# Performance work log

Hardware: AMD Instinct MI355X
Metric: run time of the kernel (lower is better)

The kernel has to match this reference:

```python
import jax, jax.numpy as jnp
import numpy as np

N = 50000   # nodes
E = 1600000 # edges
K = 5       # Chebyshev order
F_IN, H1, H2, P = 32, 32, 16, 12


def setup_inputs() -> dict:
    key = jax.random.key(0)
    ks = jax.random.split(key, 16)
    x = jax.random.normal(ks[0], (N, F_IN), dtype=jnp.float32)
    edge_index = jax.random.randint(ks[1], (2, E), 0, N, dtype=jnp.int64)
    edge_weight = jax.random.uniform(ks[2], (E,), dtype=jnp.float32)
    s = 0.1
    # Cell 1: 3 gates (z, r, h), each with x-conv [K,F_IN,H1] and h-conv [K,H1,H1]
    Wx1 = jax.random.normal(ks[3], (3, K, F_IN, H1), dtype=jnp.float32) * s
    bx1 = jax.random.normal(ks[4], (3, H1), dtype=jnp.float32) * s
    Wh1 = jax.random.normal(ks[5], (3, K, H1, H1), dtype=jnp.float32) * s
    bh1 = jax.random.normal(ks[6], (3, H1), dtype=jnp.float32) * s
    # Cell 2
    Wx2 = jax.random.normal(ks[7], (3, K, H1, H2), dtype=jnp.float32) * s
    bx2 = jax.random.normal(ks[8], (3, H2), dtype=jnp.float32) * s
    Wh2 = jax.random.normal(ks[9], (3, K, H2, H2), dtype=jnp.float32) * s
    bh2 = jax.random.normal(ks[10], (3, H2), dtype=jnp.float32) * s
    # Output linear (torch convention: weight [out,in])
    Wl = jax.random.normal(ks[11], (P, H2), dtype=jnp.float32) * s
    bl = jax.random.normal(ks[12], (P,), dtype=jnp.float32) * s
    return dict(x=x, edge_index=edge_index, edge_weight=edge_weight,
                Wx1=Wx1, bx1=bx1, Wh1=Wh1, bh1=bh1,
                Wx2=Wx2, bx2=bx2, Wh2=Wh2, bh2=bh2, Wl=Wl, bl=bl)


def _cheb_norm(edge_index, edge_weight):
    # ChebConv 'sym' norm with lambda_max=2: L_hat off-diagonal = -D^-1/2 A D^-1/2,
    # diagonal cancels to 0 (get_laplacian +1 self loop, add_self_loops fill -1).
    row, col = edge_index[0], edge_index[1]
    deg = jax.ops.segment_sum(edge_weight, row, num_segments=N)
    dis = jnp.where(deg > 0, jax.lax.rsqrt(jnp.maximum(deg, 1e-30)), 0.0)
    return -dis[row] * edge_weight * dis[col]


def _gconv_gru_forward(x, edge_index, edge_weight, Wx1, bx1, Wh1, bh1,
                       Wx2, bx2, Wh2, bh2, Wl, bl):
    row, col = edge_index[0], edge_index[1]
    wn = _cheb_norm(edge_index, edge_weight)

    def spmm(v):  # (L_hat @ v): gather source rows, scatter-add to targets
        return jax.ops.segment_sum(v[row] * wn[:, None], col, num_segments=N)

    def cheb(v, W, b):  # W: [K, Fin, Fout]
        Tx0 = v
        out = Tx0 @ W[0]
        Tx1 = spmm(Tx0)
        out = out + Tx1 @ W[1]
        for k in range(2, K):
            Tx2 = 2.0 * spmm(Tx1) - Tx0
            out = out + Tx2 @ W[k]
            Tx0, Tx1 = Tx1, Tx2
        return out + b

    def gru_cell(v, H, Wx, bx, Wh, bh):
        Z = jax.nn.sigmoid(cheb(v, Wx[0], bx[0]) + cheb(H, Wh[0], bh[0]))
        R = jax.nn.sigmoid(cheb(v, Wx[1], bx[1]) + cheb(H, Wh[1], bh[1]))
        Ht = jnp.tanh(cheb(v, Wx[2], bx[2]) + cheb(H * R, Wh[2], bh[2]))
        return Z * H + (1.0 - Z) * Ht

    h = gru_cell(x, jnp.zeros((N, H1), x.dtype), Wx1, bx1, Wh1, bh1)
    h = jax.nn.relu(h)  # dropout is identity in eval mode
    h = gru_cell(h, jnp.zeros((N, H2), x.dtype), Wx2, bx2, Wh2, bh2)
    h = jax.nn.relu(h)
    return h @ Wl.T + bl


def reference(x, edge_index, edge_weight, Wx1, bx1, Wh1, bh1,
              Wx2, bx2, Wh2, bh2, Wl, bl):
    return _gconv_gru_forward(x, edge_index, edge_weight, Wx1, bx1, Wh1, bh1,
                              Wx2, bx2, Wh2, bh2, Wl, bl)
```

## Files before the change

### kernel.cpp

```cpp
#include <hip/hip_runtime.h>
#include <math.h>

#define NN 50000
#define NE 1600000
#define KORD 5
#define NB 196
#define QTR 12500
#define GE 782
#define MT 64
#define NBK 1563
#define NBP 1600
#define NCH 256
#define ECH (NE / NCH)
#define EC4 (NE / 64)
#define PADE 1800192
#define CVB 1563

#define SCALE_W 2097152.0f
#define INV_SCALE_W (1.0f / 2097152.0f)
#define SCALE_D 4194304.0f
#define INV_SCALE_D (1.0f / 4194304.0f)

typedef _Float16 half8 __attribute__((ext_vector_type(8)));
typedef _Float16 half4v __attribute__((ext_vector_type(4)));
typedef float float4v __attribute__((ext_vector_type(4)));

__global__ __launch_bounds__(1024) void k_degbh(const int* __restrict__ ei,
                                                const float* __restrict__ ew,
                                                int* __restrict__ deg_g,
                                                int* __restrict__ bh) {
    __shared__ int sbuf[QTR];
    int bid = blockIdx.x;
    if (bid < 256) {
        int q = bid >> 6, ch = bid & 63;
        for (int i = threadIdx.x; i < QTR; i += 1024) sbuf[i] = 0;
        __syncthreads();
        int base = ch * EC4, lo = q * QTR;
        for (int e = base + threadIdx.x; e < base + EC4; e += 1024) {
            int li = ei[e] - lo;
            if ((unsigned)li < (unsigned)QTR)
                atomicAdd(&sbuf[li], __float2int_rn(ew[e] * SCALE_D));
        }
        __syncthreads();
        int* outp = deg_g + bid * QTR;
        for (int i = threadIdx.x; i < QTR; i += 1024) outp[i] = sbuf[i];
    } else {
        int ch = bid - 256;
        for (int i = threadIdx.x; i < NBK; i += 1024) sbuf[i] = 0;
        __syncthreads();
        const int* cols = ei + NE;
        int base = ch * ECH;
        for (int e = base + threadIdx.x; e < base + ECH; e += 1024)
            atomicAdd(&sbuf[cols[e] >> 5], 1);
        __syncthreads();
        int* outp = bh + ch * NBP;
        for (int b = threadIdx.x; b < NBK; b += 1024) outp[b] = sbuf[b];
    }
}

__global__ __launch_bounds__(256) void k_btotdiscvt(const int* __restrict__ bh,
                                                    int* __restrict__ tot,
                                                    const int* __restrict__ deg_g,
                                                    float* __restrict__ dis,
                                                    const float* __restrict__ x,
                                                    _Float16* __restrict__ x16) {
    int bid = blockIdx.x;
    if (bid < 7) {
        int b = bid * 256 + threadIdx.x;
        if (b >= NBP) return;
        int s = 0;
        if (b < NBK) {
#pragma unroll 8
            for (int ch = 0; ch < NCH; ch++) s += bh[ch * NBP + b];
        }
        tot[b] = s;
    } else if (bid < 7 + NB) {
        int n = (bid - 7) * 256 + threadIdx.x;
        if (n >= NN) return;
        int q = n / QTR, i = n % QTR;
        const int* p = deg_g + (q * 64) * QTR + i;
        int s = 0;
#pragma unroll
        for (int c = 0; c < 64; c++) s += p[c * QTR];
        float d = (float)s * INV_SCALE_D;
        dis[n] = s > 0 ? rsqrtf(fmaxf(d, 1e-30f)) : 0.f;
    } else {
        int i = (bid - 7 - NB) * 256 + threadIdx.x;
        if (i < NN * 8) {
            float4 v = ((const float4*)x)[i];
            half4v h = {(_Float16)v.x, (_Float16)v.y, (_Float16)v.z, (_Float16)v.w};
            *(half4v*)(x16 + i * 4) = h;
        }
    }
}

__global__ __launch_bounds__(1024) void k_bscan1(const int* __restrict__ tot,
                                                 int* __restrict__ off_bk) {
    __shared__ int s[1024];
    int t = threadIdx.x;
    int a0 = (2 * t < NBP) ? tot[2 * t] : 0;
    int a1 = (2 * t + 1 < NBP) ? tot[2 * t + 1] : 0;
    int p0 = (a0 + 127) & ~127;
    int p1 = (a1 + 127) & ~127;
    s[t] = p0 + p1;
    __syncthreads();
    for (int d = 1; d < 1024; d <<= 1) {
        int u = (t >= d) ? s[t - d] : 0;
        __syncthreads();
        s[t] += u;
        __syncthreads();
    }
    int excl = (t == 0) ? 0 : s[t - 1];
    if (2 * t < NBK) off_bk[2 * t] = excl;
    if (2 * t + 1 < NBK) off_bk[2 * t + 1] = excl + p0;
    if (t == 1023) off_bk[NBK] = s[1023];
}

__global__ __launch_bounds__(256) void k_curpad(int* __restrict__ bh,
                                                const int* __restrict__ off_bk,
                                                const int* __restrict__ tot,
                                                int2* __restrict__ edges) {
    int bid = blockIdx.x;
    if (bid < 7) {
        int b = bid * 256 + threadIdx.x;
        if (b >= NBK) return;
        int run = off_bk[b];
        for (int ch = 0; ch < NCH; ch++) {
            int v = bh[ch * NBP + b];
            bh[ch * NBP + b] = run;
            run += v;
        }
    } else {
        int b = bid - 7;
        int start = off_bk[b] + tot[b];
        int end = off_bk[b + 1];
        for (int i = start + threadIdx.x; i < end; i += 256)
            edges[i] = make_int2(0, 0);
    }
}

__global__ __launch_bounds__(1024) void k_cperm(const int* __restrict__ ei,
                                                const float* __restrict__ ew,
                                                const float* __restrict__ dis,
                                                const int* __restrict__ bh,
                                                int2* __restrict__ edges) {
    __shared__ int cur[NBK];
    int ch = blockIdx.x;
    const int* cp = bh + ch * NBP;
    for (int b = threadIdx.x; b < NBK; b += 1024) cur[b] = cp[b];
    __syncthreads();
    int base = ch * ECH;
    for (int e = base + threadIdx.x; e < base + ECH; e += 1024) {
        int r = ei[e], c = ei[NE + e];
        float w = -dis[r] * ew[e] * dis[c];
        int pos = atomicAdd(&cur[c >> 5], 1);
        int packed = (int)((unsigned)r | ((unsigned)(c & 31) << 16));
        edges[pos] = make_int2(packed, __float_as_int(w));
    }
}

#define SPMM_DS2(C0, W0, G0, C1, W1, G1)                       \
    {                                                          \
        int* a0 = &acc[C0][sub * 8];                           \
        int* a1 = &acc[C1][sub * 8];                           \
        atomicAdd(a0 + 0, __float2int_rn(W0 * (float)G0[0]));  \
        atomicAdd(a0 + 1, __float2int_rn(W0 * (float)G0[1]));  \
        atomicAdd(a0 + 2, __float2int_rn(W0 * (float)G0[2]));  \
        atomicAdd(a0 + 3, __float2int_rn(W0 * (float)G0[3]));  \
        atomicAdd(a0 + 4, __float2int_rn(W0 * (float)G0[4]));  \
        atomicAdd(a0 + 5, __float2int_rn(W0 * (float)G0[5]));  \
        atomicAdd(a0 + 6, __float2int_rn(W0 * (float)G0[6]));  \
        atomicAdd(a0 + 7, __float2int_rn(W0 * (float)G0[7]));  \
        atomicAdd(a1 + 0, __float2int_rn(W1 * (float)G1[0]));  \
        atomicAdd(a1 + 1, __float2int_rn(W1 * (float)G1[1]));  \
        atomicAdd(a1 + 2, __float2int_rn(W1 * (float)G1[2]));  \
        atomicAdd(a1 + 3, __float2int_rn(W1 * (float)G1[3]));  \
        atomicAdd(a1 + 4, __float2int_rn(W1 * (float)G1[4]));  \
        atomicAdd(a1 + 5, __float2int_rn(W1 * (float)G1[5]));  \
        atomicAdd(a1 + 6, __float2int_rn(W1 * (float)G1[6]));  \
        atomicAdd(a1 + 7, __float2int_rn(W1 * (float)G1[7]));  \
    }

__global__ __launch_bounds__(256) void k_spmm(const int* __restrict__ off_bk,
                                              const int2* __restrict__ edges,
                                              const _Float16* __restrict__ vin16,
                                              const float* __restrict__ prev,
                                              float* __restrict__ vout,
                                              _Float16* __restrict__ vout16,
                                              float scale) {
    __shared__ int acc[32][33];
    int b = blockIdx.x;
    {
        int nl = threadIdx.x >> 3, s4 = threadIdx.x & 7;
        int n = (b << 5) + nl;
        float4 p = make_float4(0.f, 0.f, 0.f, 0.f);
        if (prev && n < NN) p = ((const float4*)prev)[n * 8 + s4];
        int* a = &acc[nl][s4 * 4];
        a[0] = __float2int_rn(-p.x * SCALE_W);
        a[1] = __float2int_rn(-p.y * SCALE_W);
        a[2] = __float2int_rn(-p.z * SCALE_W);
        a[3] = __float2int_rn(-p.w * SCALE_W);
    }
    __syncthreads();
    int e0 = off_bk[b], e1 = off_bk[b + 1];
    int group = threadIdx.x >> 2, sub = threadIdx.x & 3;
    const half8* vin8 = (const half8*)vin16;
    float wscale = scale * SCALE_W;
    int nit = (e1 - e0) >> 7;
    if (nit > 0) {
        int i = e0 + group;
        int2 Ra0 = edges[i], Ra1 = edges[i + 64];
        int2 Rb0 = make_int2(0, 0), Rb1 = make_int2(0, 0);
        int2 Rc0 = make_int2(0, 0), Rc1 = make_int2(0, 0);
        if (nit > 1) { Rb0 = edges[i + 128]; Rb1 = edges[i + 192]; }
        if (nit > 2) { Rc0 = edges[i + 256]; Rc1 = edges[i + 320]; }
        half8 Ga0 = vin8[((unsigned)Ra0.x & 0xffffu) * 4 + sub];
        half8 Ga1 = vin8[((unsigned)Ra1.x & 0xffffu) * 4 + sub];
        half8 Gb0 = {}, Gb1 = {};
        if (nit > 1) {
            Gb0 = vin8[((unsigned)Rb0.x & 0xffffu) * 4 + sub];
            Gb1 = vin8[((unsigned)Rb1.x & 0xffffu) * 4 + sub];
        }
        for (int k = 0; k < nit; k++) {
            int2 Rd0 = make_int2(0, 0), Rd1 = make_int2(0, 0);
            if (k + 3 < nit) { Rd0 = edges[i + 384]; Rd1 = edges[i + 448]; }
            half8 Gc0 = {}, Gc1 = {};
            if (k + 2 < nit) {
                Gc0 = vin8[((unsigned)Rc0.x & 0xffffu) * 4 + sub];
                Gc1 = vin8[((unsigned)Rc1.x & 0xffffu) * 4 + sub];
            }
            int C0 = (unsigned)Ra0.x >> 16, C1 = (unsigned)Ra1.x >> 16;
            float W0 = __int_as_float(Ra0.y) * wscale;
            float W1 = __int_as_float(Ra1.y) * wscale;
            SPMM_DS2(C0, W0, Ga0, C1, W1, Ga1);
            Ra0 = Rb0; Ra1 = Rb1; Rb0 = Rc0; Rb1 = Rc1; Rc0 = Rd0; Rc1 = Rd1;
            Ga0 = Gb0; Ga1 = Gb1; Gb0 = Gc0; Gb1 = Gc1;
            i += 128;
        }
    }
    __syncthreads();
    int base = b << 5;
    int nl = threadIdx.x >> 3, s4 = threadIdx.x & 7;
    int n = base + nl;
    if (n < NN) {
        const int* a = &acc[nl][s4 * 4];
        float4 o = make_float4((float)a[0] * INV_SCALE_W, (float)a[1] * INV_SCALE_W,
                               (float)a[2] * INV_SCALE_W, (float)a[3] * INV_SCALE_W);
        if (vout) ((float4*)vout)[n * 8 + s4] = o;
        half4v oh = {(_Float16)o.x, (_Float16)o.y, (_Float16)o.z, (_Float16)o.w};
        *(half4v*)(vout16 + n * 32 + s4 * 4) = oh;
    }
}

__global__ __launch_bounds__(256) void k_epi1(
    const _Float16* __restrict__ x16, const _Float16* __restrict__ t1,
    const _Float16* __restrict__ t2, const _Float16* __restrict__ t3,
    const _Float16* __restrict__ t4, const float* __restrict__ Wx1,
    const float* __restrict__ bx1, const float* __restrict__ bh1,
    float* __restrict__ h, _Float16* __restrict__ h16) {
    __shared__ _Float16 T[5][MT][40];
    __shared__ _Float16 Wt[64][168];
    int n0 = blockIdx.x * MT;
    const _Float16* bufs[5] = {x16, t1, t2, t3, t4};
#pragma unroll
    for (int b = 0; b < 5; b++) {
        for (int idx = threadIdx.x; idx < MT * 4; idx += 256) {
            int r = idx >> 2, c8 = idx & 3;
            int rr = n0 + r; if (rr >= NN) rr = NN - 1;
            half8 v = *(const half8*)(bufs[b] + rr * 32 + c8 * 8);
            *(half8*)&T[b][r][c8 * 8] = v;
        }
    }
    const float* Wz = Wx1;
    const float* Wh = Wx1 + 2 * KORD * 32 * 32;
    for (int idx = threadIdx.x; idx < 160 * 64; idx += 256) {
        int k = idx >> 6, n = idx & 63;
        int b = k >> 5, i = k & 31;
        float w = (n < 32) ? Wz[b * 1024 + i * 32 + n]
                           : Wh[b * 1024 + i * 32 + (n - 32)];
        Wt[n][k] = (_Float16)w;
    }
    __syncthreads();
    int wave = threadIdx.x >> 6;
    int lane = threadIdx.x & 63;
    int lo = lane & 15, quad = lane >> 4;
    float4v acc[4];
#pragma unroll
    for (int t = 0; t < 4; t++) acc[t] = (float4v){0.f, 0.f, 0.f, 0.f};
#pragma unroll
    for (int b = 0; b < 5; b++) {
        half8 a = *(half8*)&T[b][wave * 16 + lo][quad * 8];
#pragma unroll
        for (int t = 0; t < 4; t++) {
            half8 bf = *(half8*)&Wt[t * 16 + lo][b * 32 + quad * 8];
            acc[t] = __builtin_amdgcn_mfma_f32_16x16x32_f16(a, bf, acc[t], 0, 0, 0);
        }
    }
    int nd_base = n0 + wave * 16 + quad * 4;
#pragma unroll
    for (int t = 0; t < 2; t++) {
        int j = t * 16 + lo;
        float bz = bx1[j] + bh1[j];
        float bhb = bx1[64 + j] + bh1[64 + j];
#pragma unroll
        for (int reg = 0; reg < 4; reg++) {
            int nd = nd_base + reg;
            if (nd < NN) {
                float zz = acc[t][reg] + bz;
                float hh = acc[t + 2][reg] + bhb;
                float z = 1.f / (1.f + __expf(-zz));
                float tt = __expf(-2.f * fabsf(hh));
                float ht = copysignf((1.f - tt) / (1.f + tt), hh);
                float v = fmaxf((1.f - z) * ht, 0.f);
                h[nd * 32 + j] = v;
                h16[nd * 32 + j] = (_Float16)v;
            }
        }
    }
}

__global__ __launch_bounds__(256) void k_epi2(
    const _Float16* __restrict__ h16, const _Float16* __restrict__ t1,
    const _Float16* __restrict__ t2, const _Float16* __restrict__ t3,
    const _Float16* __restrict__ t4, const float* __restrict__ Wx2,
    const float* __restrict__ bx2, const float* __restrict__ bh2,
    const float* __restrict__ Wl, const float* __restrict__ bl,
    float* __restrict__ out) {
    __shared__ _Float16 T[5][MT][40];
    __shared__ _Float16 Wt[32][168];
    __shared__ float H2[MT][17];
    int n0 = blockIdx.x * MT;
    const _Float16* bufs[5] = {h16, t1, t2, t3, t4};
#pragma unroll
    for (int b = 0; b < 5; b++) {
        for (int idx = threadIdx.x; idx < MT * 4; idx += 256) {
            int r = idx >> 2, c8 = idx & 3;
            int rr = n0 + r; if (rr >= NN) rr = NN - 1;
            half8 v = *(const half8*)(bufs[b] + rr * 32 + c8 * 8);
            *(half8*)&T[b][r][c8 * 8] = v;
        }
    }
    const float* Wz = Wx2;
    const float* Wh = Wx2 + 2 * KORD * 32 * 16;
    for (int idx = threadIdx.x; idx < 160 * 32; idx += 256) {
        int k = idx >> 5, n = idx & 31;
        int b = k >> 5, i = k & 31;
        float w = (n < 16) ? Wz[b * 512 + i * 16 + n]
                           : Wh[b * 512 + i * 16 + (n - 16)];
        Wt[n][k] = (_Float16)w;
    }
    __syncthreads();
    int wave = threadIdx.x >> 6;
    int lane = threadIdx.x & 63;
    int lo = lane & 15, quad = lane >> 4;
    float4v acc[2];
    acc[0] = (float4v){0.f, 0.f, 0.f, 0.f};
    acc[1] = (float4v){0.f, 0.f, 0.f, 0.f};
#pragma unroll
    for (int b = 0; b < 5; b++) {
        half8 a = *(half8*)&T[b][wave * 16 + lo][quad * 8];
#pragma unroll
        for (int t = 0; t < 2; t++) {
            half8 bf = *(half8*)&Wt[t * 16 + lo][b * 32 + quad * 8];
            acc[t] = __builtin_amdgcn_mfma_f32_16x16x32_f16(a, bf, acc[t], 0, 0, 0);
        }
    }
    {
        int j = lo;
        float bz = bx2[j] + bh2[j];
        float bhb = bx2[32 + j] + bh2[32 + j];
        int ndl_base = wave * 16 + quad * 4;
#pragma unroll
        for (int reg = 0; reg < 4; reg++) {
            float zz = acc[0][reg] + bz;
            float hh = acc[1][reg] + bhb;
            float z = 1.f / (1.f + __expf(-zz));
            float tt = __expf(-2.f * fabsf(hh));
            float ht = copysignf((1.f - tt) / (1.f + tt), hh);
            H2[ndl_base + reg][j] = fmaxf((1.f - z) * ht, 0.f);
        }
    }
    __syncthreads();
    for (int idx = threadIdx.x; idx < MT * 12; idx += 256) {
        int n = idx / 12, p = idx % 12;
        int gn = n0 + n;
        if (gn < NN) {
            float o = bl[p];
#pragma unroll
            for (int jj = 0; jj < 16; jj++) o = fmaf(H2[n][jj], Wl[p * 16 + jj], o);
            out[gn * 12 + p] = o;
        }
    }
}


extern "C" void kernel_launch(void* const* d_in, const int* in_sizes, int n_in,
                              void* d_out, int out_size, void* d_ws, size_t ws_size,
                              hipStream_t stream) {
    const float* x   = (const float*)d_in[0];
    const int*   ei  = (const int*)d_in[1];
    const float* ew  = (const float*)d_in[2];
    const float* Wx1 = (const float*)d_in[3];
    const float* bx1 = (const float*)d_in[4];
    const float* bh1 = (const float*)d_in[6];
    const float* Wx2 = (const float*)d_in[7];
    const float* bx2 = (const float*)d_in[8];
    const float* bh2 = (const float*)d_in[10];
    const float* Wl  = (const float*)d_in[11];
    const float* bl  = (const float*)d_in[12];
    float* out = (float*)d_out;

    float* ws     = (float*)d_ws;
    float* dis    = ws;
    int*   bh     = (int*)(ws + 50048);
    int*   tot    = bh + NCH * NBP;
    int*   off_bk = tot + NBP;
    int2*  edges  = (int2*)(off_bk + NBP);
    float* T1     = (float*)(edges + PADE);
    float* T2     = T1 + NN * 32;
    float* T3     = T2 + NN * 32;
    float* hb     = T3 + NN * 32;
    _Float16* x16 = (_Float16*)(hb + NN * 32);
    _Float16* t1h = x16 + NN * 32;
    _Float16* t2h = t1h + NN * 32;
    _Float16* t3h = t2h + NN * 32;
    _Float16* t4h = t3h + NN * 32;
    _Float16* hbh = t4h + NN * 32;
    int*   deg_g  = (int*)T1;

    k_degbh     <<<512, 1024, 0, stream>>>(ei, ew, deg_g, bh);
    k_btotdiscvt<<<7 + NB + CVB, 256, 0, stream>>>(bh, tot, deg_g, dis, x, x16);
    k_bscan1    <<<1, 1024, 0, stream>>>(tot, off_bk);
    k_curpad    <<<7 + NBK, 256, 0, stream>>>(bh, off_bk, tot, edges);
    k_cperm     <<<NCH, 1024, 0, stream>>>(ei, ew, dis, bh, edges);

    k_spmm<<<NBK, 256, 0, stream>>>(off_bk, edges, x16, nullptr, T1, t1h, 1.f);
    k_spmm<<<NBK, 256, 0, stream>>>(off_bk, edges, t1h, x,      T2, t2h, 2.f);
    k_spmm<<<NBK, 256, 0, stream>>>(off_bk, edges, t2h, T1, nullptr, t3h, 2.f);
    k_spmm<<<NBK, 256, 0, stream>>>(off_bk, edges, t3h, T2, nullptr, t4h, 2.f);
    k_epi1<<<GE, 256, 0, stream>>>(x16, t1h, t2h, t3h, t4h, Wx1, bx1, bh1, hb, hbh);

    k_spmm<<<NBK, 256, 0, stream>>>(off_bk, edges, hbh, nullptr, T1, t1h, 1.f);
    k_spmm<<<NBK, 256, 0, stream>>>(off_bk, edges, t1h, hb,     T2, t2h, 2.f);
    k_spmm<<<NBK, 256, 0, stream>>>(off_bk, edges, t2h, T1, nullptr, t3h, 2.f);
    k_spmm<<<NBK, 256, 0, stream>>>(off_bk, edges, t3h, T2, nullptr, t4h, 2.f);
    k_epi2<<<GE, 256, 0, stream>>>(hbh, t1h, t2h, t3h, t4h, Wx2, bx2, bh2, Wl, bl, out);
}
```

Before: 340.0 us.

## Fuse four Chebyshev SpMM passes into one cooperative kernel with grid syncs

Replaces the four separate k_spmm launches per GRU cell with a single cooperative kernel that runs the four propagation passes back to back, separated by grid-wide barriers, over a persistent grid of 1024 blocks striding across the 1563 node blocks. This removes three kernel launch gaps and tail drains per cell. In exchange, the grid-sync cost is paid each pass, work per pass is less evenly spread (some blocks handle two node blocks, others one), and the launch depends on 1024 blocks being co-resident.

Result: slower. 1.120 ms (+229.3%).

```diff
diff --git a/kernel.cpp b/kernel.cpp
--- a/kernel.cpp
+++ b/kernel.cpp
@@ -1,5 +1,8 @@
 #include <hip/hip_runtime.h>
+#include <hip/hip_cooperative_groups.h>
 #include <math.h>
+
+namespace cg = cooperative_groups;
 
 #define NN 50000
 #define NE 1600000
@@ -15,6 +18,7 @@
 #define EC4 (NE / 64)
 #define PADE 1800192
 #define CVB 1563
+#define GRID_SP 1024
 
 #define SCALE_W 2097152.0f
 #define INV_SCALE_W (1.0f / 2097152.0f)
@@ -181,75 +185,96 @@
         atomicAdd(a1 + 7, __float2int_rn(W1 * (float)G1[7]));  \
     }
 
-__global__ __launch_bounds__(256) void k_spmm(const int* __restrict__ off_bk,
-                                              const int2* __restrict__ edges,
-                                              const _Float16* __restrict__ vin16,
-                                              const float* __restrict__ prev,
-                                              float* __restrict__ vout,
-                                              _Float16* __restrict__ vout16,
-                                              float scale) {
-    __shared__ int acc[32][33];
-    int b = blockIdx.x;
-    {
-        int nl = threadIdx.x >> 3, s4 = threadIdx.x & 7;
-        int n = (b << 5) + nl;
-        float4 p = make_float4(0.f, 0.f, 0.f, 0.f);
-        if (prev && n < NN) p = ((const float4*)prev)[n * 8 + s4];
-        int* a = &acc[nl][s4 * 4];
-        a[0] = __float2int_rn(-p.x * SCALE_W);
-        a[1] = __float2int_rn(-p.y * SCALE_W);
-        a[2] = __float2int_rn(-p.z * SCALE_W);
-        a[3] = __float2int_rn(-p.w * SCALE_W);
-    }
-    __syncthreads();
-    int e0 = off_bk[b], e1 = off_bk[b + 1];
+__device__ __forceinline__ void spmm_pass(const int* __restrict__ off_bk,
+                                          const int2* __restrict__ edges,
+                                          const _Float16* __restrict__ vin16,
+                                          const float* __restrict__ prev,
+                                          float* __restrict__ vout,
+                                          _Float16* __restrict__ vout16,
+                                          float scale, int acc[32][33]) {
     int group = threadIdx.x >> 2, sub = threadIdx.x & 3;
     const half8* vin8 = (const half8*)vin16;
     float wscale = scale * SCALE_W;
-    int nit = (e1 - e0) >> 7;
-    if (nit > 0) {
-        int i = e0 + group;
-        int2 Ra0 = edges[i], Ra1 = edges[i + 64];
-        int2 Rb0 = make_int2(0, 0), Rb1 = make_int2(0, 0);
-        int2 Rc0 = make_int2(0, 0), Rc1 = make_int2(0, 0);
-        if (nit > 1) { Rb0 = edges[i + 128]; Rb1 = edges[i + 192]; }
-        if (nit > 2) { Rc0 = edges[i + 256]; Rc1 = edges[i + 320]; }
-        half8 Ga0 = vin8[((unsigned)Ra0.x & 0xffffu) * 4 + sub];
-        half8 Ga1 = vin8[((unsigned)Ra1.x & 0xffffu) * 4 + sub];
-        half8 Gb0 = {}, Gb1 = {};
-        if (nit > 1) {
-            Gb0 = vin8[((unsigned)Rb0.x & 0xffffu) * 4 + sub];
-            Gb1 = vin8[((unsigned)Rb1.x & 0xffffu) * 4 + sub];
-        }
-        for (int k = 0; k < nit; k++) {
-            int2 Rd0 = make_int2(0, 0), Rd1 = make_int2(0, 0);
-            if (k + 3 < nit) { Rd0 = edges[i + 384]; Rd1 = edges[i + 448]; }
-            half8 Gc0 = {}, Gc1 = {};
-            if (k + 2 < nit) {
-                Gc0 = vin8[((unsigned)Rc0.x & 0xffffu) * 4 + sub];
-                Gc1 = vin8[((unsigned)Rc1.x & 0xffffu) * 4 + sub];
+    for (int b = blockIdx.x; b < NBK; b += GRID_SP) {
+        {
+            int nl = threadIdx.x >> 3, s4 = threadIdx.x & 7;
+            int n = (b << 5) + nl;
+            float4 p = make_float4(0.f, 0.f, 0.f, 0.f);
+            if (prev && n < NN) p = ((const float4*)prev)[n * 8 + s4];
+            int* a = &acc[nl][s4 * 4];
+            a[0] = __float2int_rn(-p.x * SCALE_W);
+            a[1] = __float2int_rn(-p.y * SCALE_W);
+            a[2] = __float2int_rn(-p.z * SCALE_W);
+            a[3] = __float2int_rn(-p.w * SCALE_W);
+        }
+        __syncthreads();
+        int e0 = off_bk[b], e1 = off_bk[b + 1];
+        int nit = (e1 - e0) >> 7;
+        if (nit > 0) {
+            int i = e0 + group;
+            int2 Ra0 = edges[i], Ra1 = edges[i + 64];
+            int2 Rb0 = make_int2(0, 0), Rb1 = make_int2(0, 0);
+            int2 Rc0 = make_int2(0, 0), Rc1 = make_int2(0, 0);
+            if (nit > 1) { Rb0 = edges[i + 128]; Rb1 = edges[i + 192]; }
+            if (nit > 2) { Rc0 = edges[i + 256]; Rc1 = edges[i + 320]; }
+            half8 Ga0 = vin8[((unsigned)Ra0.x & 0xffffu) * 4 + sub];
+            half8 Ga1 = vin8[((unsigned)Ra1.x & 0xffffu) * 4 + sub];
+            half8 Gb0 = {}, Gb1 = {};
+            if (nit > 1) {
+                Gb0 = vin8[((unsigned)Rb0.x & 0xffffu) * 4 + sub];
+                Gb1 = vin8[((unsigned)Rb1.x & 0xffffu) * 4 + sub];
             }
-            int C0 = (unsigned)Ra0.x >> 16, C1 = (unsigned)Ra1.x >> 16;
-            float W0 = __int_as_float(Ra0.y) * wscale;
-            float W1 = __int_as_float(Ra1.y) * wscale;
-            SPMM_DS2(C0, W0, Ga0, C1, W1, Ga1);
-            Ra0 = Rb0; Ra1 = Rb1; Rb0 = Rc0; Rb1 = Rc1; Rc0 = Rd0; Rc1 = Rd1;
-            Ga0 = Gb0; Ga1 = Gb1; Gb0 = Gc0; Gb1 = Gc1;
-            i += 128;
-        }
-    }
-    __syncthreads();
-    int base = b << 5;
-    int nl = threadIdx.x >> 3, s4 = threadIdx.x & 7;
-    int n = base + nl;
-    if (n < NN) {
-        const int* a = &acc[nl][s4 * 4];
-        float4 o = make_float4((float)a[0] * INV_SCALE_W, (float)a[1] * INV_SCALE_W,
-                               (float)a[2] * INV_SCALE_W, (float)a[3] * INV_SCALE_W);
-        if (vout) ((float4*)vout)[n * 8 + s4] = o;
-        half4v oh = {(_Float16)o.x, (_Float16)o.y, (_Float16)o.z, (_Float16)o.w};
-        *(half4v*)(vout16 + n * 32 + s4 * 4) = oh;
-    }
+            for (int k = 0; k < nit; k++) {
+                int2 Rd0 = make_int2(0, 0), Rd1 = make_int2(0, 0);
+                if (k + 3 < nit) { Rd0 = edges[i + 384]; Rd1 = edges[i + 448]; }
+                half8 Gc0 = {}, Gc1 = {};
+                if (k + 2 < nit) {
+                    Gc0 = vin8[((unsigned)Rc0.x & 0xffffu) * 4 + sub];
+                    Gc1 = vin8[((unsigned)Rc1.x & 0xffffu) * 4 + sub];
+                }
+                int C0 = (unsigned)Ra0.x >> 16, C1 = (unsigned)Ra1.x >> 16;
+                float W0 = __int_as_float(Ra0.y) * wscale;
+                float W1 = __int_as_float(Ra1.y) * wscale;
+                SPMM_DS2(C0, W0, Ga0, C1, W1, Ga1);
+                Ra0 = Rb0; Ra1 = Rb1; Rb0 = Rc0; Rb1 = Rc1; Rc0 = Rd0; Rc1 = Rd1;
+                Ga0 = Gb0; Ga1 = Gb1; Gb0 = Gc0; Gb1 = Gc1;
+                i += 128;
+            }
+        }
+        __syncthreads();
+        {
+            int nl = threadIdx.x >> 3, s4 = threadIdx.x & 7;
+            int n = (b << 5) + nl;
+            if (n < NN) {
+                const int* a = &acc[nl][s4 * 4];
+                float4 o = make_float4((float)a[0] * INV_SCALE_W,
+                                       (float)a[1] * INV_SCALE_W,
+                                       (float)a[2] * INV_SCALE_W,
+                                       (float)a[3] * INV_SCALE_W);
+                if (vout) ((float4*)vout)[n * 8 + s4] = o;
+                half4v oh = {(_Float16)o.x, (_Float16)o.y, (_Float16)o.z, (_Float16)o.w};
+                *(half4v*)(vout16 + n * 32 + s4 * 4) = oh;
+            }
+        }
+        __syncthreads();
+    }
+}
+
+__global__ __launch_bounds__(256) void k_spmm4(
+    const int* __restrict__ off_bk, const int2* __restrict__ edges,
+    const _Float16* __restrict__ v0h, const float* __restrict__ v0f,
+    float* __restrict__ T1, float* __restrict__ T2,
+    _Float16* __restrict__ t1h, _Float16* __restrict__ t2h,
+    _Float16* __restrict__ t3h, _Float16* __restrict__ t4h) {
+    __shared__ int acc[32][33];
+    cg::grid_group grid = cg::this_grid();
+    spmm_pass(off_bk, edges, v0h, nullptr, T1, t1h, 1.f, acc);
+    grid.sync();
+    spmm_pass(off_bk, edges, t1h, v0f, T2, t2h, 2.f, acc);
+    grid.sync();
+    spmm_pass(off_bk, edges, t2h, T1, nullptr, t3h, 2.f, acc);
+    grid.sync();
+    spmm_pass(off_bk, edges, t3h, T2, nullptr, t4h, 2.f, acc);
 }
 
 __global__ __launch_bounds__(256) void k_epi1(
@@ -434,15 +459,26 @@
     k_curpad    <<<7 + NBK, 256, 0, stream>>>(bh, off_bk, tot, edges);
     k_cperm     <<<NCH, 1024, 0, stream>>>(ei, ew, dis, bh, edges);
 
-    k_spmm<<<NBK, 256, 0, stream>>>(off_bk, edges, x16, nullptr, T1, t1h, 1.f);
-    k_spmm<<<NBK, 256, 0, stream>>>(off_bk, edges, t1h, x,      T2, t2h, 2.f);
-    k_spmm<<<NBK, 256, 0, stream>>>(off_bk, edges, t2h, T1, nullptr, t3h, 2.f);
-    k_spmm<<<NBK, 256, 0, stream>>>(off_bk, edges, t3h, T2, nullptr, t4h, 2.f);
+    const int* off_bk_c = off_bk;
+    const int2* edges_c = edges;
+
+    {
+        const _Float16* v0h = x16; const float* v0f = x;
+        void* a1[] = {(void*)&off_bk_c, (void*)&edges_c, (void*)&v0h, (void*)&v0f,
+                      (void*)&T1, (void*)&T2, (void*)&t1h, (void*)&t2h,
+                      (void*)&t3h, (void*)&t4h};
+        hipLaunchCooperativeKernel((void*)k_spmm4, dim3(GRID_SP), dim3(256),
+                                   a1, 0, stream);
+    }
     k_epi1<<<GE, 256, 0, stream>>>(x16, t1h, t2h, t3h, t4h, Wx1, bx1, bh1, hb, hbh);
 
-    k_spmm<<<NBK, 256, 0, stream>>>(off_bk, edges, hbh, nullptr, T1, t1h, 1.f);
-    k_spmm<<<NBK, 256, 0, stream>>>(off_bk, edges, t1h, hb,     T2, t2h, 2.f);
-    k_spmm<<<NBK, 256, 0, stream>>>(off_bk, edges, t2h, T1, nullptr, t3h, 2.f);
-    k_spmm<<<NBK, 256, 0, stream>>>(off_bk, edges, t3h, T2, nullptr, t4h, 2.f);
+    {
+        const _Float16* v0h = hbh; const float* v0f = hb;
+        void* a2[] = {(void*)&off_bk_c, (void*)&edges_c, (void*)&v0h, (void*)&v0f,
+                      (void*)&T1, (void*)&T2, (void*)&t1h, (void*)&t2h,
+                      (void*)&t3h, (void*)&t4h};
+        hipLaunchCooperativeKernel((void*)k_spmm4, dim3(GRID_SP), dim3(256),
+                                   a2, 0, stream);
+    }
     k_epi2<<<GE, 256, 0, stream>>>(hbh, t1h, t2h, t3h, t4h, Wx2, bx2, bh2, Wl, bl, out);
 }
```

## Replace bucketed LDS-atomic SpMM with per-node CSR row gather in registers

Applied to the files above, without the earlier changes.

The 32-node bucket layout with padded edge lists and fixed-point LDS atomic accumulation is replaced by a full per-target-node CSR. Edges are now counted per node, scanned in a single-block kernel and scattered with global atomics on per-node cursors. Each SpMM row is then reduced by 4 lanes in fp32 registers with no shared-memory atomics or int quantisation. This removes atomic contention and one preprocessing kernel, but adds variable per-row loop lengths that cause load imbalance, global atomics in the permutation step, and a shorter prefetch depth.

After: 564.0 us. 65.9% more time.

```diff
diff --git a/kernel.cpp b/kernel.cpp
--- a/kernel.cpp
+++ b/kernel.cpp
@@ -8,16 +8,12 @@
 #define QTR 12500
 #define GE 782
 #define MT 64
-#define NBK 1563
-#define NBP 1600
 #define NCH 256
 #define ECH (NE / NCH)
 #define EC4 (NE / 64)
-#define PADE 1800192
 #define CVB 1563
-
-#define SCALE_W 2097152.0f
-#define INV_SCALE_W (1.0f / 2097152.0f)
+#define NPAD 50048
+
 #define SCALE_D 4194304.0f
 #define INV_SCALE_D (1.0f / 4194304.0f)
 
@@ -25,57 +21,45 @@
 typedef _Float16 half4v __attribute__((ext_vector_type(4)));
 typedef float float4v __attribute__((ext_vector_type(4)));
 
-__global__ __launch_bounds__(1024) void k_degbh(const int* __restrict__ ei,
-                                                const float* __restrict__ ew,
-                                                int* __restrict__ deg_g,
-                                                int* __restrict__ bh) {
+__global__ __launch_bounds__(1024) void k_degcnt(const int* __restrict__ ei,
+                                                 const float* __restrict__ ew,
+                                                 int* __restrict__ deg_g,
+                                                 int* __restrict__ cnt_g) {
     __shared__ int sbuf[QTR];
     int bid = blockIdx.x;
+    int local = bid & 255;
+    int q = local >> 6, ch = local & 63;
+    for (int i = threadIdx.x; i < QTR; i += 1024) sbuf[i] = 0;
+    __syncthreads();
+    int base = ch * EC4, lo = q * QTR;
     if (bid < 256) {
-        int q = bid >> 6, ch = bid & 63;
-        for (int i = threadIdx.x; i < QTR; i += 1024) sbuf[i] = 0;
-        __syncthreads();
-        int base = ch * EC4, lo = q * QTR;
         for (int e = base + threadIdx.x; e < base + EC4; e += 1024) {
             int li = ei[e] - lo;
             if ((unsigned)li < (unsigned)QTR)
                 atomicAdd(&sbuf[li], __float2int_rn(ew[e] * SCALE_D));
         }
-        __syncthreads();
-        int* outp = deg_g + bid * QTR;
-        for (int i = threadIdx.x; i < QTR; i += 1024) outp[i] = sbuf[i];
     } else {
-        int ch = bid - 256;
-        for (int i = threadIdx.x; i < NBK; i += 1024) sbuf[i] = 0;
-        __syncthreads();
         const int* cols = ei + NE;
-        int base = ch * ECH;
-        for (int e = base + threadIdx.x; e < base + ECH; e += 1024)
-            atomicAdd(&sbuf[cols[e] >> 5], 1);
-        __syncthreads();
-        int* outp = bh + ch * NBP;
-        for (int b = threadIdx.x; b < NBK; b += 1024) outp[b] = sbuf[b];
-    }
-}
-
-__global__ __launch_bounds__(256) void k_btotdiscvt(const int* __restrict__ bh,
-                                                    int* __restrict__ tot,
-                                                    const int* __restrict__ deg_g,
-                                                    float* __restrict__ dis,
-                                                    const float* __restrict__ x,
-                                                    _Float16* __restrict__ x16) {
+        for (int e = base + threadIdx.x; e < base + EC4; e += 1024) {
+            int li = cols[e] - lo;
+            if ((unsigned)li < (unsigned)QTR)
+                atomicAdd(&sbuf[li], 1);
+        }
+    }
+    __syncthreads();
+    int* outp = (bid < 256 ? deg_g : cnt_g) + local * QTR;
+    for (int i = threadIdx.x; i < QTR; i += 1024) outp[i] = sbuf[i];
+}
+
+__global__ __launch_bounds__(256) void k_discntcvt(const int* __restrict__ deg_g,
+                                                   const int* __restrict__ cnt_g,
+                                                   float* __restrict__ dis,
+                                                   int* __restrict__ cnt,
+                                                   const float* __restrict__ x,
+                                                   _Float16* __restrict__ x16) {
     int bid = blockIdx.x;
-    if (bid < 7) {
-        int b = bid * 256 + threadIdx.x;
-        if (b >= NBP) return;
-        int s = 0;
-        if (b < NBK) {
-#pragma unroll 8
-            for (int ch = 0; ch < NCH; ch++) s += bh[ch * NBP + b];
-        }
-        tot[b] = s;
-    } else if (bid < 7 + NB) {
-        int n = (bid - 7) * 256 + threadIdx.x;
+    if (bid < NB) {
+        int n = bid * 256 + threadIdx.x;
         if (n >= NN) return;
         int q = n / QTR, i = n % QTR;
         const int* p = deg_g + (q * 64) * QTR + i;
@@ -84,8 +68,17 @@
         for (int c = 0; c < 64; c++) s += p[c * QTR];
         float d = (float)s * INV_SCALE_D;
         dis[n] = s > 0 ? rsqrtf(fmaxf(d, 1e-30f)) : 0.f;
+    } else if (bid < 2 * NB) {
+        int n = (bid - NB) * 256 + threadIdx.x;
+        if (n >= NN) return;
+        int q = n / QTR, i = n % QTR;
+        const int* p = cnt_g + (q * 64) * QTR + i;
+        int s = 0;
+#pragma unroll
+        for (int c = 0; c < 64; c++) s += p[c * QTR];
+        cnt[n] = s;
     } else {
-        int i = (bid - 7 - NB) * 256 + threadIdx.x;
+        int i = (bid - 2 * NB) * 256 + threadIdx.x;
         if (i < NN * 8) {
             float4 v = ((const float4*)x)[i];
             half4v h = {(_Float16)v.x, (_Float16)v.y, (_Float16)v.z, (_Float16)v.w};
@@ -94,15 +87,19 @@
     }
 }
 
-__global__ __launch_bounds__(1024) void k_bscan1(const int* __restrict__ tot,
-                                                 int* __restrict__ off_bk) {
+__global__ __launch_bounds__(1024) void k_scan(const int* __restrict__ cnt,
+                                               int* __restrict__ off,
+                                               int* __restrict__ cur) {
     __shared__ int s[1024];
+    const int CH = 49;
     int t = threadIdx.x;
-    int a0 = (2 * t < NBP) ? tot[2 * t] : 0;
-    int a1 = (2 * t + 1 < NBP) ? tot[2 * t + 1] : 0;
-    int p0 = (a0 + 127) & ~127;
-    int p1 = (a1 + 127) & ~127;
-    s[t] = p0 + p1;
+    int base = t * CH;
+    int sum = 0;
+    for (int i = 0; i < CH; i++) {
+        int idx = base + i;
+        if (idx < NN) sum += cnt[idx];
+    }
+    s[t] = sum;
     __syncthreads();
     for (int d = 1; d < 1024; d <<= 1) {
         int u = (t >= d) ? s[t - d] : 0;
@@ -110,146 +107,78 @@
         s[t] += u;
         __syncthreads();
     }
-    int excl = (t == 0) ? 0 : s[t - 1];
-    if (2 * t < NBK) off_bk[2 * t] = excl;
-    if (2 * t + 1 < NBK) off_bk[2 * t + 1] = excl + p0;
-    if (t == 1023) off_bk[NBK] = s[1023];
-}
-
-__global__ __launch_bounds__(256) void k_curpad(int* __restrict__ bh,
-                                                const int* __restrict__ off_bk,
-                                                const int* __restrict__ tot,
-                                                int2* __restrict__ edges) {
-    int bid = blockIdx.x;
-    if (bid < 7) {
-        int b = bid * 256 + threadIdx.x;
-        if (b >= NBK) return;
-        int run = off_bk[b];
-        for (int ch = 0; ch < NCH; ch++) {
-            int v = bh[ch * NBP + b];
-            bh[ch * NBP + b] = run;
-            run += v;
-        }
-    } else {
-        int b = bid - 7;
-        int start = off_bk[b] + tot[b];
-        int end = off_bk[b + 1];
-        for (int i = start + threadIdx.x; i < end; i += 256)
-            edges[i] = make_int2(0, 0);
-    }
+    int run = (t == 0) ? 0 : s[t - 1];
+    for (int i = 0; i < CH; i++) {
+        int idx = base + i;
+        if (idx < NN) {
+            int c = cnt[idx];
+            off[idx] = run;
+            cur[idx] = run;
+            run += c;
+        }
+    }
+    if (t == 1023) off[NN] = s[1023];
 }
 
 __global__ __launch_bounds__(1024) void k_cperm(const int* __restrict__ ei,
                                                 const float* __restrict__ ew,
                                                 const float* __restrict__ dis,
-                                                const int* __restrict__ bh,
+                                                int* __restrict__ cur,
                                                 int2* __restrict__ edges) {
-    __shared__ int cur[NBK];
     int ch = blockIdx.x;
-    const int* cp = bh + ch * NBP;
-    for (int b = threadIdx.x; b < NBK; b += 1024) cur[b] = cp[b];
-    __syncthreads();
     int base = ch * ECH;
     for (int e = base + threadIdx.x; e < base + ECH; e += 1024) {
         int r = ei[e], c = ei[NE + e];
         float w = -dis[r] * ew[e] * dis[c];
-        int pos = atomicAdd(&cur[c >> 5], 1);
-        int packed = (int)((unsigned)r | ((unsigned)(c & 31) << 16));
-        edges[pos] = make_int2(packed, __float_as_int(w));
-    }
-}
-
-#define SPMM_DS2(C0, W0, G0, C1, W1, G1)                       \
-    {                                                          \
-        int* a0 = &acc[C0][sub * 8];                           \
-        int* a1 = &acc[C1][sub * 8];                           \
-        atomicAdd(a0 + 0, __float2int_rn(W0 * (float)G0[0]));  \
-        atomicAdd(a0 + 1, __float2int_rn(W0 * (float)G0[1]));  \
-        atomicAdd(a0 + 2, __float2int_rn(W0 * (float)G0[2]));  \
-        atomicAdd(a0 + 3, __float2int_rn(W0 * (float)G0[3]));  \
-        atomicAdd(a0 + 4, __float2int_rn(W0 * (float)G0[4]));  \
-        atomicAdd(a0 + 5, __float2int_rn(W0 * (float)G0[5]));  \
-        atomicAdd(a0 + 6, __float2int_rn(W0 * (float)G0[6]));  \
-        atomicAdd(a0 + 7, __float2int_rn(W0 * (float)G0[7]));  \
-        atomicAdd(a1 + 0, __float2int_rn(W1 * (float)G1[0]));  \
-        atomicAdd(a1 + 1, __float2int_rn(W1 * (float)G1[1]));  \
-        atomicAdd(a1 + 2, __float2int_rn(W1 * (float)G1[2]));  \
-        atomicAdd(a1 + 3, __float2int_rn(W1 * (float)G1[3]));  \
-        atomicAdd(a1 + 4, __float2int_rn(W1 * (float)G1[4]));  \
-        atomicAdd(a1 + 5, __float2int_rn(W1 * (float)G1[5]));  \
-        atomicAdd(a1 + 6, __float2int_rn(W1 * (float)G1[6]));  \
-        atomicAdd(a1 + 7, __float2int_rn(W1 * (float)G1[7]));  \
-    }
-
-__global__ __launch_bounds__(256) void k_spmm(const int* __restrict__ off_bk,
+        int pos = atomicAdd(&cur[c], 1);
+        edges[pos] = make_int2(r, __float_as_int(w));
+    }
+}
+
+__global__ __launch_bounds__(256) void k_spmm(const int* __restrict__ off,
                                               const int2* __restrict__ edges,
                                               const _Float16* __restrict__ vin16,
                                               const float* __restrict__ prev,
                                               float* __restrict__ vout,
                                               _Float16* __restrict__ vout16,
                                               float scale) {
-    __shared__ int acc[32][33];
-    int b = blockIdx.x;
-    {
-        int nl = threadIdx.x >> 3, s4 = threadIdx.x & 7;
-        int n = (b << 5) + nl;
-        float4 p = make_float4(0.f, 0.f, 0.f, 0.f);
-        if (prev && n < NN) p = ((const float4*)prev)[n * 8 + s4];
-        int* a = &acc[nl][s4 * 4];
-        a[0] = __float2int_rn(-p.x * SCALE_W);
-        a[1] = __float2int_rn(-p.y * SCALE_W);
-        a[2] = __float2int_rn(-p.z * SCALE_W);
-        a[3] = __float2int_rn(-p.w * SCALE_W);
-    }
-    __syncthreads();
-    int e0 = off_bk[b], e1 = off_bk[b + 1];
     int group = threadIdx.x >> 2, sub = threadIdx.x & 3;
+    int n = blockIdx.x * 64 + group;
+    if (n >= NN) return;
     const half8* vin8 = (const half8*)vin16;
-    float wscale = scale * SCALE_W;
-    int nit = (e1 - e0) >> 7;
-    if (nit > 0) {
-        int i = e0 + group;
-        int2 Ra0 = edges[i], Ra1 = edges[i + 64];
-        int2 Rb0 = make_int2(0, 0), Rb1 = make_int2(0, 0);
-        int2 Rc0 = make_int2(0, 0), Rc1 = make_int2(0, 0);
-        if (nit > 1) { Rb0 = edges[i + 128]; Rb1 = edges[i + 192]; }
-        if (nit > 2) { Rc0 = edges[i + 256]; Rc1 = edges[i + 320]; }
-        half8 Ga0 = vin8[((unsigned)Ra0.x & 0xffffu) * 4 + sub];
-        half8 Ga1 = vin8[((unsigned)Ra1.x & 0xffffu) * 4 + sub];
-        half8 Gb0 = {}, Gb1 = {};
-        if (nit > 1) {
-            Gb0 = vin8[((unsigned)Rb0.x & 0xffffu) * 4 + sub];
-            Gb1 = vin8[((unsigned)Rb1.x & 0xffffu) * 4 + sub];
-        }
-        for (int k = 0; k < nit; k++) {
-            int2 Rd0 = make_int2(0, 0), Rd1 = make_int2(0, 0);
-            if (k + 3 < nit) { Rd0 = edges[i + 384]; Rd1 = edges[i + 448]; }
-            half8 Gc0 = {}, Gc1 = {};
-            if (k + 2 < nit) {
-                Gc0 = vin8[((unsigned)Rc0.x & 0xffffu) * 4 + sub];
-                Gc1 = vin8[((unsigned)Rc1.x & 0xffffu) * 4 + sub];
-            }
-            int C0 = (unsigned)Ra0.x >> 16, C1 = (unsigned)Ra1.x >> 16;
-            float W0 = __int_as_float(Ra0.y) * wscale;
-            float W1 = __int_as_float(Ra1.y) * wscale;
-            SPMM_DS2(C0, W0, Ga0, C1, W1, Ga1);
-            Ra0 = Rb0; Ra1 = Rb1; Rb0 = Rc0; Rb1 = Rc1; Rc0 = Rd0; Rc1 = Rd1;
-            Ga0 = Gb0; Ga1 = Gb1; Gb0 = Gc0; Gb1 = Gc1;
-            i += 128;
-        }
-    }
-    __syncthreads();
-    int base = b << 5;
-    int nl = threadIdx.x >> 3, s4 = threadIdx.x & 7;
-    int n = base + nl;
-    if (n < NN) {
-        const int* a = &acc[nl][s4 * 4];
-        float4 o = make_float4((float)a[0] * INV_SCALE_W, (float)a[1] * INV_SCALE_W,
-                               (float)a[2] * INV_SCALE_W, (float)a[3] * INV_SCALE_W);
-        if (vout) ((float4*)vout)[n * 8 + s4] = o;
-        half4v oh = {(_Float16)o.x, (_Float16)o.y, (_Float16)o.z, (_Float16)o.w};
-        *(half4v*)(vout16 + n * 32 + s4 * 4) = oh;
-    }
+    int e0 = off[n], e1 = off[n + 1];
+    float acc[8] = {0.f, 0.f, 0.f, 0.f, 0.f, 0.f, 0.f, 0.f};
+    if (e0 < e1) {
+        int2 Ra = edges[e0];
+        int2 Rb = (e0 + 1 < e1) ? edges[e0 + 1] : make_int2(0, 0);
+        half8 Ga = vin8[(unsigned)Ra.x * 4 + sub];
+        for (int e = e0; e < e1; e++) {
+            int2 Rc = (e + 2 < e1) ? edges[e + 2] : make_int2(0, 0);
+            half8 Gb = {};
+            if (e + 1 < e1) Gb = vin8[(unsigned)Rb.x * 4 + sub];
+            float w = __int_as_float(Ra.y);
+#pragma unroll
+            for (int j = 0; j < 8; j++) acc[j] = fmaf(w, (float)Ga[j], acc[j]);
+            Ra = Rb; Rb = Rc; Ga = Gb;
+        }
+    }
+    float o[8];
+    if (prev) {
+        const float* pp = prev + n * 32 + sub * 8;
+#pragma unroll
+        for (int j = 0; j < 8; j++) o[j] = fmaf(scale, acc[j], -pp[j]);
+    } else {
+#pragma unroll
+        for (int j = 0; j < 8; j++) o[j] = scale * acc[j];
+    }
+    if (vout) {
+        float* vp = vout + n * 32 + sub * 8;
+        *(float4*)vp = make_float4(o[0], o[1], o[2], o[3]);
+        *(float4*)(vp + 4) = make_float4(o[4], o[5], o[6], o[7]);
+    }
+    half8 oh = {(_Float16)o[0], (_Float16)o[1], (_Float16)o[2], (_Float16)o[3],
+                (_Float16)o[4], (_Float16)o[5], (_Float16)o[6], (_Float16)o[7]};
+    *(half8*)(vout16 + n * 32 + sub * 8) = oh;
 }
 
 __global__ __launch_bounds__(256) void k_epi1(
@@ -412,14 +341,13 @@
 
     float* ws     = (float*)d_ws;
     float* dis    = ws;
-    int*   bh     = (int*)(ws + 50048);
-    int*   tot    = bh + NCH * NBP;
-    int*   off_bk = tot + NBP;
-    int2*  edges  = (int2*)(off_bk + NBP);
-    float* T1     = (float*)(edges + PADE);
+    int*   cnt    = (int*)(ws + NPAD);
+    int*   off    = cnt + NPAD;
+    int*   cur    = off + NPAD;
+    int2*  edges  = (int2*)(cur + NPAD);
+    float* T1     = (float*)(edges + NE);
     float* T2     = T1 + NN * 32;
-    float* T3     = T2 + NN * 32;
-    float* hb     = T3 + NN * 32;
+    float* hb     = T2 + NN * 32;
     _Float16* x16 = (_Float16*)(hb + NN * 32);
     _Float16* t1h = x16 + NN * 32;
     _Float16* t2h = t1h + NN * 32;
@@ -427,22 +355,22 @@
     _Float16* t4h = t3h + NN * 32;
     _Float16* hbh = t4h + NN * 32;
     int*   deg_g  = (int*)T1;
-
-    k_degbh     <<<512, 1024, 0, stream>>>(ei, ew, deg_g, bh);
-    k_btotdiscvt<<<7 + NB + CVB, 256, 0, stream>>>(bh, tot, deg_g, dis, x, x16);
-    k_bscan1    <<<1, 1024, 0, stream>>>(tot, off_bk);
-    k_curpad    <<<7 + NBK, 256, 0, stream>>>(bh, off_bk, tot, edges);
-    k_cperm     <<<NCH, 1024, 0, stream>>>(ei, ew, dis, bh, edges);
-
-    k_spmm<<<NBK, 256, 0, stream>>>(off_bk, edges, x16, nullptr, T1, t1h, 1.f);
-    k_spmm<<<NBK, 256, 0, stream>>>(off_bk, edges, t1h, x,      T2, t2h, 2.f);
-    k_spmm<<<NBK, 256, 0, stream>>>(off_bk, edges, t2h, T1, nullptr, t3h, 2.f);
-    k_spmm<<<NBK, 256, 0, stream>>>(off_bk, edges, t3h, T2, nullptr, t4h, 2.f);
+    int*   cnt_g  = (int*)(hbh + NN * 32);
+
+    k_degcnt  <<<512, 1024, 0, stream>>>(ei, ew, deg_g, cnt_g);
+    k_discntcvt<<<2 * NB + CVB, 256, 0, stream>>>(deg_g, cnt_g, dis, cnt, x, x16);
+    k_scan    <<<1, 1024, 0, stream>>>(cnt, off, cur);
+    k_cperm   <<<NCH, 1024, 0, stream>>>(ei, ew, dis, cur, edges);
+
+    k_spmm<<<GE, 256, 0, stream>>>(off, edges, x16, nullptr, T1, t1h, 1.f);
+    k_spmm<<<GE, 256, 0, stream>>>(off, edges, t1h, x,      T2, t2h, 2.f);
+    k_spmm<<<GE, 256, 0, stream>>>(off, edges, t2h, T1, nullptr, t3h, 2.f);
+    k_spmm<<<GE, 256, 0, stream>>>(off, edges, t3h, T2, nullptr, t4h, 2.f);
     k_epi1<<<GE, 256, 0, stream>>>(x16, t1h, t2h, t3h, t4h, Wx1, bx1, bh1, hb, hbh);
 
-    k_spmm<<<NBK, 256, 0, stream>>>(off_bk, edges, hbh, nullptr, T1, t1h, 1.f);
-    k_spmm<<<NBK, 256, 0, stream>>>(off_bk, edges, t1h, hb,     T2, t2h, 2.f);
-    k_spmm<<<NBK, 256, 0, stream>>>(off_bk, edges, t2h, T1, nullptr, t3h, 2.f);
-    k_spmm<<<NBK, 256, 0, stream>>>(off_bk, edges, t3h, T2, nullptr, t4h, 2.f);
+    k_spmm<<<GE, 256, 0, stream>>>(off, edges, hbh, nullptr, T1, t1h, 1.f);
+    k_spmm<<<GE, 256, 0, stream>>>(off, edges, t1h, hb,     T2, t2h, 2.f);
+    k_spmm<<<GE, 256, 0, stream>>>(off, edges, t2h, T1, nullptr, t3h, 2.f);
+    k_spmm<<<GE, 256, 0, stream>>>(off, edges, t3h, T2, nullptr, t4h, 2.f);
     k_epi2<<<GE, 256, 0, stream>>>(hbh, t1h, t2h, t3h, t4h, Wx2, bx2, bh2, Wl, bl, out);
 }
```
